# Optimization experiments

Measured on AMD Instinct MI355X. Metric: run time of the kernel, lower is better.

The kernel has to match this reference:

```python
import jax, jax.numpy as jnp
import numpy as np

T = 4096      # tokens
H = 1024      # hidden_size
I = 4096      # intermediate_size
E = 8         # num_experts


def setup_inputs() -> dict:
    key = jax.random.key(0)
    ks = jax.random.split(key, 6)
    s_h = 1.0 / np.sqrt(H)
    s_i = 1.0 / np.sqrt(I)
    return {
        "x":  jax.random.normal(ks[0], (T, H), dtype=jnp.float32),
        "Wg": jax.random.uniform(ks[1], (E, H), jnp.float32, -s_h, s_h),   # gate: Linear(H, E), no bias
        "W1": jax.random.uniform(ks[2], (E, H, I), jnp.float32, -s_h, s_h),
        "b1": jax.random.uniform(ks[3], (E, I), jnp.float32, -s_h, s_h),
        "W2": jax.random.uniform(ks[4], (E, I, H), jnp.float32, -s_i, s_i),
        "b2": jax.random.uniform(ks[5], (E, H), jnp.float32, -s_i, s_i),
    }


def reference(x, Wg, W1, b1, W2, b2):
    # Gate: softmax over experts. gate_scores: [T, E]
    gate_scores = jax.nn.softmax(x @ Wg.T, axis=-1)
    # All experts run densely on all tokens (batched GEMMs).
    h = jax.nn.gelu(jnp.einsum('th,ehi->eti', x, W1) + b1[:, None, :],
                    approximate=False)                      # [E, T, I]
    y = jnp.einsum('eti,eih->eth', h, W2) + b2[:, None, :]  # [E, T, H]
    # Gate-weighted sum over experts (fuses the stack + mul + sum).
    return jnp.einsum('te,eth->th', gate_scores, y)         # [T, H]
```

## Files before the change

kernel.cpp:

```cpp
#include <hip/hip_runtime.h>
#include <math.h>

#define T_TOK 4096
#define H_DIM 1024
#define I_DIM 4096
#define E_NUM 8


typedef short s16x8 __attribute__((ext_vector_type(8)));
typedef float f32x4 __attribute__((ext_vector_type(4)));

__device__ __forceinline__ unsigned short f2b(float f) {
  union { float f; unsigned u; } v; v.f = f;
  unsigned r = v.u + 0x7fffu + ((v.u >> 16) & 1u);
  return (unsigned short)(r >> 16);
}

__device__ __forceinline__ void gld_lds16(short* lds, const short* g) {
  __builtin_amdgcn_global_load_lds(
      (const __attribute__((address_space(1))) void*)g,
      (__attribute__((address_space(3))) void*)lds, 16, 0, 0);
}

__device__ __forceinline__ float gelu_f(float v) {
  float a = fabsf(v);
  float z = a * 0.70710678118f;
  float t = __builtin_amdgcn_rcpf(fmaf(0.47047f, z, 1.0f));
  float p = fmaf(fmaf(0.7478556f, t, -0.0958798f), t, 0.3480242f) * t;
  float e = __expf(-z * z);
  float erf_abs = fmaf(-p, e, 1.0f);
  return fmaf(0.5f * a, erf_abs, 0.5f * v);
}

__global__ __launch_bounds__(256) void gate_kernel(
    const float* __restrict__ x, const float* __restrict__ Wg,
    float* __restrict__ gate)
{
  int t = blockIdx.x * 4 + (threadIdx.x >> 6);
  int lane = threadIdx.x & 63;
  const float* xr = x + (size_t)t * H_DIM;
  float acc[E_NUM];
#pragma unroll
  for (int e = 0; e < E_NUM; ++e) acc[e] = 0.f;
  for (int j = 0; j < H_DIM / 64; ++j) {
    float xv = xr[lane + j * 64];
#pragma unroll
    for (int e = 0; e < E_NUM; ++e)
      acc[e] += xv * Wg[e * H_DIM + lane + j * 64];
  }
#pragma unroll
  for (int e = 0; e < E_NUM; ++e)
    for (int s = 32; s > 0; s >>= 1)
      acc[e] += __shfl_xor(acc[e], s, 64);
  if (lane == 0) {
    float mx = acc[0];
#pragma unroll
    for (int e = 1; e < E_NUM; ++e) mx = fmaxf(mx, acc[e]);
    float sum = 0.f, ex[E_NUM];
#pragma unroll
    for (int e = 0; e < E_NUM; ++e) { ex[e] = expf(acc[e] - mx); sum += ex[e]; }
    float inv = 1.f / sum;
#pragma unroll
    for (int e = 0; e < E_NUM; ++e) gate[t * E_NUM + e] = ex[e] * inv;
  }
}

__global__ __launch_bounds__(256) void convert_x_kernel(
    const float* __restrict__ x, short* __restrict__ xb)
{
  int idx = blockIdx.x * 256 + threadIdx.x;
  int t = idx >> 7;
  int h0 = (idx & 127) << 3;
  const float* src = x + (size_t)t * H_DIM + h0;
  float4 a = *(const float4*)src;
  float4 b = *(const float4*)(src + 4);
  s16x8 v;
  v[0] = f2b(a.x); v[1] = f2b(a.y); v[2] = f2b(a.z); v[3] = f2b(a.w);
  v[4] = f2b(b.x); v[5] = f2b(b.y); v[6] = f2b(b.z); v[7] = f2b(b.w);
  int rb = t >> 8, kt = h0 >> 6, half = (t >> 7) & 1;
  size_t off = ((size_t)((rb * 16 + kt) * 2 + half)) * 8192
             + (size_t)(t & 127) * 64 + (h0 & 63);
  *(s16x8*)(xb + off) = v;
}

__global__ __launch_bounds__(256) void trans_w1_kernel(
    const float* __restrict__ W1, short* __restrict__ W1t)
{
  __shared__ short tile[64][65];
  const int e = blockIdx.z;
  const int i0 = blockIdx.x * 64, h0 = blockIdx.y * 64;
  const int tid = threadIdx.x, c = tid & 63, r0 = tid >> 6;
  const float* src = W1 + ((size_t)e * H_DIM + h0) * I_DIM + i0;
#pragma unroll
  for (int j = 0; j < 16; ++j) {
    int r = j * 4 + r0;
    tile[r][c] = f2b(src[(size_t)r * I_DIM + c]);
  }
  __syncthreads();
  const int i = tid & 63, kq = tid >> 6;
  const size_t base = ((size_t)((e * 16 + (i0 >> 8)) * 16 + (h0 >> 6)) * 2
                       + ((i0 >> 7) & 1)) * 8192
                    + (size_t)((i0 & 64) + i) * 64;
#pragma unroll
  for (int w = 0; w < 2; ++w) {
    int kcl = kq + w * 4;
    s16x8 v;
#pragma unroll
    for (int j = 0; j < 8; ++j) v[j] = tile[kcl * 8 + j][i];
    *(s16x8*)(W1t + base + kcl * 8) = v;
  }
}

__global__ __launch_bounds__(256) void trans_w2_kernel(
    const float* __restrict__ W2, short* __restrict__ W2t)
{
  __shared__ short tile[64][65];
  const int e = blockIdx.z;
  const int i0 = blockIdx.x * 64, h0 = blockIdx.y * 64;
  const int tid = threadIdx.x, c = tid & 63, r0 = tid >> 6;
  const float* src = W2 + ((size_t)e * I_DIM + i0) * H_DIM + h0;
#pragma unroll
  for (int j = 0; j < 16; ++j) {
    int r = j * 4 + r0;
    tile[r][c] = f2b(src[(size_t)r * H_DIM + c]);
  }
  __syncthreads();
  const int h = tid & 63, kq = tid >> 6;
  const size_t base = ((size_t)((h0 >> 8) * 512 + e * 64 + (i0 >> 6)) * 2
                       + ((h0 >> 7) & 1)) * 8192
                    + (size_t)((h0 & 64) + h) * 64;
#pragma unroll
  for (int w = 0; w < 2; ++w) {
    int kcl = kq + w * 4;
    s16x8 v;
#pragma unroll
    for (int j = 0; j < 8; ++j) v[j] = tile[kcl * 8 + j][h];
    *(s16x8*)(W2t + base + kcl * 8) = v;
  }
}


#define BARR()  __builtin_amdgcn_s_barrier()
#define FENCE() asm volatile("" ::: "memory")
#define LGKM0() do { asm volatile("s_waitcnt lgkmcnt(0)" ::: "memory"); \
                     __builtin_amdgcn_sched_barrier(0); } while (0)
#define VMC(N)  asm volatile("s_waitcnt vmcnt(" #N ")" ::: "memory")
#define PRIO1() __builtin_amdgcn_s_setprio(1)
#define PRIO0() __builtin_amdgcn_s_setprio(0)
#define SCHEDB() __builtin_amdgcn_sched_barrier(0)

__device__ __forceinline__ void gemm_core(
    const short* __restrict__ Ag, const short* __restrict__ Bg,
    int nk, short* lds, f32x4 acc[8][4])
{
  const int tid  = threadIdx.x;
  const int wave = tid >> 6, lane = tid & 63;
  const int wm = wave >> 2, wn = wave & 3;
  const int g = lane >> 4, r16 = lane & 15;

  const int L0 = tid * 16;
  const int L1 = 8192 + tid * 16;
  const int s0 = (L0 ^ (((L0 >> 7) & 7) << 4)) >> 1;
  const int s1 = (L1 ^ (((L1 >> 7) & 7) << 4)) >> 1;

  short* stA = lds + wave * 512;
  short* stB = lds + 32768 + wave * 512;

  const int xr_ = (r16 & 7) << 4;
  const int rd0 = r16 * 64 + ((((0 << 6) | (g << 4)) ^ xr_) >> 1);
  const int rd1 = r16 * 64 + ((((1 << 6) | (g << 4)) ^ xr_) >> 1);

  const short* Ah = lds + wm * 8192;
  const short* Bh = lds + 32768 + (wn >> 1) * 8192 + (wn & 1) * 4096;

  s16x8 af[16], bf0, bf1;

#define STAGE_A(KT, HH, BUF) do { \
    const short* _s = Ag + (size_t)(KT) * 16384 + (HH) * 8192; \
    short* _d = stA + ((BUF) * 2 + (HH)) * 8192; \
    gld_lds16(_d, _s + s0); \
    gld_lds16(_d + 4096, _s + s1); } while (0)
#define STAGE_B(KT, HH, BUF) do { \
    const short* _s = Bg + (size_t)(KT) * 16384 + (HH) * 8192; \
    short* _d = stB + ((BUF) * 2 + (HH)) * 8192; \
    gld_lds16(_d, _s + s0); \
    gld_lds16(_d + 4096, _s + s1); } while (0)
#define LDA(BUF) \
    _Pragma("unroll") \
    for (int mi = 0; mi < 8; ++mi) { \
      af[mi * 2]     = *(const s16x8*)(Ah + (BUF) * 16384 + mi * 1024 + rd0); \
      af[mi * 2 + 1] = *(const s16x8*)(Ah + (BUF) * 16384 + mi * 1024 + rd1); }
#define LDB(BUF, NL) do { \
    bf0 = *(const s16x8*)(Bh + (BUF) * 16384 + (NL) * 1024 + rd0); \
    bf1 = *(const s16x8*)(Bh + (BUF) * 16384 + (NL) * 1024 + rd1); } while (0)
#define MFMA_COL(NL) \
    _Pragma("unroll") \
    for (int mi = 0; mi < 8; ++mi) { \
      acc[mi][NL] = __builtin_amdgcn_mfma_f32_16x16x32_bf16(af[mi * 2], bf0, acc[mi][NL], 0, 0, 0); \
      acc[mi][NL] = __builtin_amdgcn_mfma_f32_16x16x32_bf16(af[mi * 2 + 1], bf1, acc[mi][NL], 0, 0, 0); }

  STAGE_A(0, 0, 0); STAGE_A(0, 1, 0); STAGE_B(0, 0, 0); STAGE_B(0, 1, 0);
  STAGE_A(1, 0, 1); STAGE_A(1, 1, 1);
  VMC(4);
  BARR(); FENCE();

  const int iters = nk >> 1;
  for (int it = 0; it < iters; ++it) {
    const int u = it * 2, v = u + 1;
    const bool nlast = (it + 1 < iters);

    LDA(0); LDB(0, 0);
    STAGE_B(v, 0, 1);
    BARR(); LGKM0();
    PRIO1(); MFMA_COL(0); PRIO0();
    SCHEDB(); BARR(); FENCE();

    LDB(0, 1);
    STAGE_B(v, 1, 1);
    BARR(); LGKM0();
    PRIO1(); MFMA_COL(1); PRIO0();
    SCHEDB(); BARR(); FENCE();

    LDB(0, 2);
    if (nlast) STAGE_A(u + 2, 0, 0);
    BARR(); LGKM0();
    PRIO1(); MFMA_COL(2); PRIO0();
    SCHEDB(); BARR(); FENCE();

    LDB(0, 3);
    if (nlast) STAGE_A(u + 2, 1, 0);
    BARR(); LGKM0();
    PRIO1(); MFMA_COL(3); PRIO0();
    if (nlast) { VMC(4); } else { VMC(0); }
    SCHEDB(); BARR(); FENCE();

    LDA(1); LDB(1, 0);
    if (nlast) STAGE_B(u + 2, 0, 0);
    BARR(); LGKM0();
    PRIO1(); MFMA_COL(0); PRIO0();
    SCHEDB(); BARR(); FENCE();

    LDB(1, 1);
    if (nlast) STAGE_B(u + 2, 1, 0);
    BARR(); LGKM0();
    PRIO1(); MFMA_COL(1); PRIO0();
    SCHEDB(); BARR(); FENCE();

    LDB(1, 2);
    if (nlast) STAGE_A(v + 2, 0, 1);
    BARR(); LGKM0();
    PRIO1(); MFMA_COL(2); PRIO0();
    SCHEDB(); BARR(); FENCE();

    LDB(1, 3);
    if (nlast) STAGE_A(v + 2, 1, 1);
    BARR(); LGKM0();
    PRIO1(); MFMA_COL(3); PRIO0();
    if (nlast) VMC(4);
    SCHEDB(); BARR(); FENCE();
  }
#undef STAGE_A
#undef STAGE_B
#undef LDA
#undef LDB
#undef MFMA_COL
}

__global__ __launch_bounds__(512) void gemm1_kernel(
    const short* __restrict__ xb, const short* __restrict__ W1t,
    const float* __restrict__ b1, const float* __restrict__ gate,
    short* __restrict__ hg)
{
  extern __shared__ short lds[];
  const int bi = blockIdx.x, bt = blockIdx.y, e = blockIdx.z;
  f32x4 acc[8][4];
#pragma unroll
  for (int i = 0; i < 8; ++i)
#pragma unroll
    for (int j = 0; j < 4; ++j) acc[i][j] = (f32x4){0.f, 0.f, 0.f, 0.f};

  const short* Ag = W1t + (size_t)(e * 16 + bi) * 16 * 16384;
  const short* Bg = xb + (size_t)bt * 16 * 16384;
  gemm_core(Ag, Bg, 16, lds, acc);

  const int tid = threadIdx.x, wave = tid >> 6, lane = tid & 63;
  const int wm = wave >> 2, wn = wave & 3, g = lane >> 4, r16 = lane & 15;
#pragma unroll
  for (int mg = 0; mg < 8; ++mg) {
    const int i4 = bi * 256 + wm * 128 + mg * 16 + g * 4;
    const float4 b1v = *(const float4*)(b1 + e * I_DIM + i4);
    const int kt = (e * I_DIM + i4) >> 6;
    const int c = i4 & 63;
    short* dst = hg + ((size_t)(bt * 512 + kt) * 2 + (wn >> 1)) * 8192 + c;
#pragma unroll
    for (int ng = 0; ng < 4; ++ng) {
      const int tl = wn * 64 + ng * 16 + r16;
      const float gt = gate[(bt * 256 + tl) * E_NUM + e];
      const float v0 = gelu_f(acc[mg][ng][0] + b1v.x) * gt;
      const float v1 = gelu_f(acc[mg][ng][1] + b1v.y) * gt;
      const float v2 = gelu_f(acc[mg][ng][2] + b1v.z) * gt;
      const float v3 = gelu_f(acc[mg][ng][3] + b1v.w) * gt;
      int2 pk;
      pk.x = (int)((unsigned)f2b(v0) | ((unsigned)f2b(v1) << 16));
      pk.y = (int)((unsigned)f2b(v2) | ((unsigned)f2b(v3) << 16));
      *(int2*)(dst + (size_t)(tl & 127) * 64) = pk;
    }
  }
}

__global__ __launch_bounds__(512) void gemm2_kernel(
    const short* __restrict__ W2t, const short* __restrict__ hg,
    float* __restrict__ part)
{
  extern __shared__ short lds[];
  const int bh = blockIdx.x, bt = blockIdx.y, ks = blockIdx.z;
  f32x4 acc[8][4];
#pragma unroll
  for (int i = 0; i < 8; ++i)
#pragma unroll
    for (int j = 0; j < 4; ++j) acc[i][j] = (f32x4){0.f, 0.f, 0.f, 0.f};

  const short* Ag = W2t + (size_t)(bh * 512 + ks * 128) * 16384;
  const short* Bg = hg  + (size_t)(bt * 512 + ks * 128) * 16384;
  gemm_core(Ag, Bg, 128, lds, acc);

  const int tid = threadIdx.x, wave = tid >> 6, lane = tid & 63;
  const int wm = wave >> 2, wn = wave & 3, g = lane >> 4, r16 = lane & 15;
  float* dst = part + (size_t)ks * ((size_t)T_TOK * H_DIM);
#pragma unroll
  for (int mg = 0; mg < 8; ++mg) {
    const int h4 = bh * 256 + wm * 128 + mg * 16 + g * 4;
#pragma unroll
    for (int ng = 0; ng < 4; ++ng) {
      const int t = bt * 256 + wn * 64 + ng * 16 + r16;
      *(f32x4*)(dst + (size_t)t * H_DIM + h4) = acc[mg][ng];
    }
  }
}

__global__ __launch_bounds__(256) void reduce_kernel(
    const float* __restrict__ part, const float* __restrict__ gate,
    const float* __restrict__ b2, float* __restrict__ out)
{
  const int idx = blockIdx.x * 256 + threadIdx.x;
  const int t = idx >> 8;
  const int h4 = (idx & 255) << 2;
  const size_t off = (size_t)t * H_DIM + h4;
  const size_t SL = (size_t)T_TOK * H_DIM;
  float4 a0 = *(const float4*)(part + off);
  float4 a1 = *(const float4*)(part + SL + off);
  float4 a2 = *(const float4*)(part + 2 * SL + off);
  float4 a3 = *(const float4*)(part + 3 * SL + off);
  float sx = a0.x + a1.x + a2.x + a3.x;
  float sy = a0.y + a1.y + a2.y + a3.y;
  float sz = a0.z + a1.z + a2.z + a3.z;
  float sw = a0.w + a1.w + a2.w + a3.w;
#pragma unroll
  for (int e = 0; e < E_NUM; ++e) {
    const float gv = gate[t * E_NUM + e];
    const float4 bv = *(const float4*)(b2 + e * H_DIM + h4);
    sx = fmaf(gv, bv.x, sx); sy = fmaf(gv, bv.y, sy);
    sz = fmaf(gv, bv.z, sz); sw = fmaf(gv, bv.w, sw);
  }
  float4 r; r.x = sx; r.y = sy; r.z = sz; r.w = sw;
  *(float4*)(out + off) = r;
}

extern "C" void kernel_launch(void* const* d_in, const int* in_sizes, int n_in,
                              void* d_out, int out_size, void* d_ws, size_t ws_size,
                              hipStream_t stream) {
  const float* x  = (const float*)d_in[0];
  const float* Wg = (const float*)d_in[1];
  const float* W1 = (const float*)d_in[2];
  const float* b1 = (const float*)d_in[3];
  const float* W2 = (const float*)d_in[4];
  const float* b2 = (const float*)d_in[5];
  float* out = (float*)d_out;

  char* ws = (char*)d_ws;
  float* gate = (float*)ws;
  short* xb   = (short*)(ws + 131072);
  short* W1t  = (short*)(ws + 131072 + 8388608);
  short* W2t  = (short*)(ws + 131072 + 8388608 + 67108864);
  short* hg   = (short*)(ws + 131072 + 8388608 + 2 * 67108864);
  float* part = (float*)(ws + 131072);

  static bool attr_done = false;
  if (!attr_done) {
    hipFuncSetAttribute((const void*)gemm1_kernel,
                        hipFuncAttributeMaxDynamicSharedMemorySize, 131072);
    hipFuncSetAttribute((const void*)gemm2_kernel,
                        hipFuncAttributeMaxDynamicSharedMemorySize, 131072);
    attr_done = true;
  }

  gate_kernel<<<T_TOK / 4, 256, 0, stream>>>(x, Wg, gate);
  convert_x_kernel<<<2048, 256, 0, stream>>>(x, xb);
  trans_w1_kernel<<<dim3(I_DIM / 64, H_DIM / 64, E_NUM), 256, 0, stream>>>(W1, W1t);
  trans_w2_kernel<<<dim3(I_DIM / 64, H_DIM / 64, E_NUM), 256, 0, stream>>>(W2, W2t);
  gemm1_kernel<<<dim3(16, 16, 8), 512, 131072, stream>>>(xb, W1t, b1, gate, hg);
  gemm2_kernel<<<dim3(4, 16, 4), 512, 131072, stream>>>(W2t, hg, part);
  reduce_kernel<<<4096, 256, 0, stream>>>(part, gate, b2, out);
}
```

Baseline: 893.8 us.

## Rewrite GEMMs with 128x128 tiles, 4-stage pipeline, 2 blocks per CU

Replaces the 256x256, 512-thread GEMM core with 128x128 tiles over 256 threads and a k=32 packed layout. A 4-deep global-to-LDS ring buffer uses one barrier per k-step, and launch bounds allow two blocks per CU. All weight and activation transforms switch to 32-wide k chunks. gemm1 now loops over all experts inside one block, reusing the x tile from cache, and gemm2 drops split-K from 4 to 2, so the reduce kernel sums fewer partials. The intent is better occupancy and latency hiding, at the cost of lower per-block arithmetic intensity and more LDS traffic per MFMA.

```diff
diff --git a/kernel.cpp b/kernel.cpp
--- a/kernel.cpp
+++ b/kernel.cpp
@@ -77,9 +77,8 @@
   s16x8 v;
   v[0] = f2b(a.x); v[1] = f2b(a.y); v[2] = f2b(a.z); v[3] = f2b(a.w);
   v[4] = f2b(b.x); v[5] = f2b(b.y); v[6] = f2b(b.z); v[7] = f2b(b.w);
-  int rb = t >> 8, kt = h0 >> 6, half = (t >> 7) & 1;
-  size_t off = ((size_t)((rb * 16 + kt) * 2 + half)) * 8192
-             + (size_t)(t & 127) * 64 + (h0 & 63);
+  size_t off = ((size_t)((t >> 7) * 32 + (h0 >> 5))) * 4096
+             + (size_t)(t & 127) * 32 + (h0 & 31);
   *(s16x8*)(xb + off) = v;
 }
 
@@ -98,16 +97,15 @@
   }
   __syncthreads();
   const int i = tid & 63, kq = tid >> 6;
-  const size_t base = ((size_t)((e * 16 + (i0 >> 8)) * 16 + (h0 >> 6)) * 2
-                       + ((i0 >> 7) & 1)) * 8192
-                    + (size_t)((i0 & 64) + i) * 64;
 #pragma unroll
   for (int w = 0; w < 2; ++w) {
     int kcl = kq + w * 4;
     s16x8 v;
 #pragma unroll
     for (int j = 0; j < 8; ++j) v[j] = tile[kcl * 8 + j][i];
-    *(s16x8*)(W1t + base + kcl * 8) = v;
+    size_t off = (((size_t)e * 32 + (i0 >> 7)) * 32 + (h0 >> 5) + (kcl >> 2)) * 4096
+               + (size_t)((i0 & 64) + i) * 32 + (kcl & 3) * 8;
+    *(s16x8*)(W1t + off) = v;
   }
 }
 
@@ -126,16 +124,15 @@
   }
   __syncthreads();
   const int h = tid & 63, kq = tid >> 6;
-  const size_t base = ((size_t)((h0 >> 8) * 512 + e * 64 + (i0 >> 6)) * 2
-                       + ((h0 >> 7) & 1)) * 8192
-                    + (size_t)((h0 & 64) + h) * 64;
 #pragma unroll
   for (int w = 0; w < 2; ++w) {
     int kcl = kq + w * 4;
     s16x8 v;
 #pragma unroll
     for (int j = 0; j < 8; ++j) v[j] = tile[kcl * 8 + j][h];
-    *(s16x8*)(W2t + base + kcl * 8) = v;
+    size_t off = ((size_t)(h0 >> 7) * 1024 + e * 128 + (i0 >> 5) + (kcl >> 2)) * 4096
+               + (size_t)((h0 & 64) + h) * 32 + (kcl & 3) * 8;
+    *(s16x8*)(W2t + off) = v;
   }
 }
 
@@ -148,192 +145,178 @@
 #define PRIO1() __builtin_amdgcn_s_setprio(1)
 #define PRIO0() __builtin_amdgcn_s_setprio(0)
 #define SCHEDB() __builtin_amdgcn_sched_barrier(0)
-
-__device__ __forceinline__ void gemm_core(
-    const short* __restrict__ Ag, const short* __restrict__ Bg,
-    int nk, short* lds, f32x4 acc[8][4])
-{
-  const int tid  = threadIdx.x;
-  const int wave = tid >> 6, lane = tid & 63;
-  const int wm = wave >> 2, wn = wave & 3;
-  const int g = lane >> 4, r16 = lane & 15;
-
-  const int L0 = tid * 16;
-  const int L1 = 8192 + tid * 16;
-  const int s0 = (L0 ^ (((L0 >> 7) & 7) << 4)) >> 1;
-  const int s1 = (L1 ^ (((L1 >> 7) & 7) << 4)) >> 1;
-
-  short* stA = lds + wave * 512;
-  short* stB = lds + 32768 + wave * 512;
-
-  const int xr_ = (r16 & 7) << 4;
-  const int rd0 = r16 * 64 + ((((0 << 6) | (g << 4)) ^ xr_) >> 1);
-  const int rd1 = r16 * 64 + ((((1 << 6) | (g << 4)) ^ xr_) >> 1);
-
-  const short* Ah = lds + wm * 8192;
-  const short* Bh = lds + 32768 + (wn >> 1) * 8192 + (wn & 1) * 4096;
-
-  s16x8 af[16], bf0, bf1;
-
-#define STAGE_A(KT, HH, BUF) do { \
-    const short* _s = Ag + (size_t)(KT) * 16384 + (HH) * 8192; \
-    short* _d = stA + ((BUF) * 2 + (HH)) * 8192; \
-    gld_lds16(_d, _s + s0); \
-    gld_lds16(_d + 4096, _s + s1); } while (0)
-#define STAGE_B(KT, HH, BUF) do { \
-    const short* _s = Bg + (size_t)(KT) * 16384 + (HH) * 8192; \
-    short* _d = stB + ((BUF) * 2 + (HH)) * 8192; \
-    gld_lds16(_d, _s + s0); \
-    gld_lds16(_d + 4096, _s + s1); } while (0)
-#define LDA(BUF) \
-    _Pragma("unroll") \
-    for (int mi = 0; mi < 8; ++mi) { \
-      af[mi * 2]     = *(const s16x8*)(Ah + (BUF) * 16384 + mi * 1024 + rd0); \
-      af[mi * 2 + 1] = *(const s16x8*)(Ah + (BUF) * 16384 + mi * 1024 + rd1); }
-#define LDB(BUF, NL) do { \
-    bf0 = *(const s16x8*)(Bh + (BUF) * 16384 + (NL) * 1024 + rd0); \
-    bf1 = *(const s16x8*)(Bh + (BUF) * 16384 + (NL) * 1024 + rd1); } while (0)
-#define MFMA_COL(NL) \
-    _Pragma("unroll") \
-    for (int mi = 0; mi < 8; ++mi) { \
-      acc[mi][NL] = __builtin_amdgcn_mfma_f32_16x16x32_bf16(af[mi * 2], bf0, acc[mi][NL], 0, 0, 0); \
-      acc[mi][NL] = __builtin_amdgcn_mfma_f32_16x16x32_bf16(af[mi * 2 + 1], bf1, acc[mi][NL], 0, 0, 0); }
-
-  STAGE_A(0, 0, 0); STAGE_A(0, 1, 0); STAGE_B(0, 0, 0); STAGE_B(0, 1, 0);
-  STAGE_A(1, 0, 1); STAGE_A(1, 1, 1);
-  VMC(4);
-  BARR(); FENCE();
-
-  const int iters = nk >> 1;
-  for (int it = 0; it < iters; ++it) {
-    const int u = it * 2, v = u + 1;
-    const bool nlast = (it + 1 < iters);
-
-    LDA(0); LDB(0, 0);
-    STAGE_B(v, 0, 1);
-    BARR(); LGKM0();
-    PRIO1(); MFMA_COL(0); PRIO0();
-    SCHEDB(); BARR(); FENCE();
-
-    LDB(0, 1);
-    STAGE_B(v, 1, 1);
-    BARR(); LGKM0();
-    PRIO1(); MFMA_COL(1); PRIO0();
-    SCHEDB(); BARR(); FENCE();
-
-    LDB(0, 2);
-    if (nlast) STAGE_A(u + 2, 0, 0);
-    BARR(); LGKM0();
-    PRIO1(); MFMA_COL(2); PRIO0();
-    SCHEDB(); BARR(); FENCE();
-
-    LDB(0, 3);
-    if (nlast) STAGE_A(u + 2, 1, 0);
-    BARR(); LGKM0();
-    PRIO1(); MFMA_COL(3); PRIO0();
-    if (nlast) { VMC(4); } else { VMC(0); }
-    SCHEDB(); BARR(); FENCE();
-
-    LDA(1); LDB(1, 0);
-    if (nlast) STAGE_B(u + 2, 0, 0);
-    BARR(); LGKM0();
-    PRIO1(); MFMA_COL(0); PRIO0();
-    SCHEDB(); BARR(); FENCE();
-
-    LDB(1, 1);
-    if (nlast) STAGE_B(u + 2, 1, 0);
-    BARR(); LGKM0();
-    PRIO1(); MFMA_COL(1); PRIO0();
-    SCHEDB(); BARR(); FENCE();
-
-    LDB(1, 2);
-    if (nlast) STAGE_A(v + 2, 0, 1);
-    BARR(); LGKM0();
-    PRIO1(); MFMA_COL(2); PRIO0();
-    SCHEDB(); BARR(); FENCE();
-
-    LDB(1, 3);
-    if (nlast) STAGE_A(v + 2, 1, 1);
-    BARR(); LGKM0();
-    PRIO1(); MFMA_COL(3); PRIO0();
-    if (nlast) VMC(4);
-    SCHEDB(); BARR(); FENCE();
-  }
-#undef STAGE_A
-#undef STAGE_B
-#undef LDA
-#undef LDB
-#undef MFMA_COL
-}
-
-__global__ __launch_bounds__(512) void gemm1_kernel(
+#define MF(A, B, C) __builtin_amdgcn_mfma_f32_16x16x32_bf16(A, B, C, 0, 0, 0)
+
+__global__ __launch_bounds__(256, 2) void gemm1_kernel(
     const short* __restrict__ xb, const short* __restrict__ W1t,
     const float* __restrict__ b1, const float* __restrict__ gate,
     short* __restrict__ hg)
 {
   extern __shared__ short lds[];
-  const int bi = blockIdx.x, bt = blockIdx.y, e = blockIdx.z;
-  f32x4 acc[8][4];
-#pragma unroll
-  for (int i = 0; i < 8; ++i)
+  const int bi = blockIdx.x, bt = blockIdx.y;
+  const int tid = threadIdx.x, wave = tid >> 6, lane = tid & 63;
+  const int wm = wave >> 1, wn = wave & 1;
+  const int g = lane >> 4, r16 = lane & 15;
+
+  const int D0 = (wave * 2) * 1024 + lane * 16;
+  const int D1 = (wave * 2 + 1) * 1024 + lane * 16;
+  const int s0 = (D0 ^ (((D0 >> 6) & 3) << 4)) >> 1;
+  const int s1 = (D1 ^ (((D1 >> 6) & 3) << 4)) >> 1;
+  short* dA0 = lds + (wave * 2) * 512;
+  short* dA1 = lds + (wave * 2 + 1) * 512;
+  short* dB0 = lds + 16384 + (wave * 2) * 512;
+  short* dB1 = lds + 16384 + (wave * 2 + 1) * 512;
+
+  const int rdf = r16 * 32 + ((g << 3) ^ ((r16 & 3) << 3));
+  const short* Ah = lds + (wm * 64) * 32;
+  const short* Bh = lds + 16384 + (wn * 64) * 32;
+
+  const short* Bw = xb + (size_t)bt * 32 * 4096;
+
+  f32x4 acc[4][4];
+#pragma unroll
+  for (int i = 0; i < 4; ++i)
 #pragma unroll
     for (int j = 0; j < 4; ++j) acc[i][j] = (f32x4){0.f, 0.f, 0.f, 0.f};
 
-  const short* Ag = W1t + (size_t)(e * 16 + bi) * 16 * 16384;
-  const short* Bg = xb + (size_t)bt * 16 * 16384;
-  gemm_core(Ag, Bg, 16, lds, acc);
-
-  const int tid = threadIdx.x, wave = tid >> 6, lane = tid & 63;
-  const int wm = wave >> 2, wn = wave & 3, g = lane >> 4, r16 = lane & 15;
-#pragma unroll
-  for (int mg = 0; mg < 8; ++mg) {
-    const int i4 = bi * 256 + wm * 128 + mg * 16 + g * 4;
-    const float4 b1v = *(const float4*)(b1 + e * I_DIM + i4);
-    const int kt = (e * I_DIM + i4) >> 6;
-    const int c = i4 & 63;
-    short* dst = hg + ((size_t)(bt * 512 + kt) * 2 + (wn >> 1)) * 8192 + c;
-#pragma unroll
-    for (int ng = 0; ng < 4; ++ng) {
-      const int tl = wn * 64 + ng * 16 + r16;
-      const float gt = gate[(bt * 256 + tl) * E_NUM + e];
-      const float v0 = gelu_f(acc[mg][ng][0] + b1v.x) * gt;
-      const float v1 = gelu_f(acc[mg][ng][1] + b1v.y) * gt;
-      const float v2 = gelu_f(acc[mg][ng][2] + b1v.z) * gt;
-      const float v3 = gelu_f(acc[mg][ng][3] + b1v.w) * gt;
-      int2 pk;
-      pk.x = (int)((unsigned)f2b(v0) | ((unsigned)f2b(v1) << 16));
-      pk.y = (int)((unsigned)f2b(v2) | ((unsigned)f2b(v3) << 16));
-      *(int2*)(dst + (size_t)(tl & 127) * 64) = pk;
+#define STAGE1(KK) do { \
+    const int _c = ((KK) >> 5) * 1024 + bi * 32 + ((KK) & 31); \
+    const short* _sa = W1t + (size_t)_c * 4096; \
+    const short* _sb = Bw + (size_t)((KK) & 31) * 4096; \
+    const int _o = ((KK) & 3) * 4096; \
+    gld_lds16(dA0 + _o, _sa + s0); \
+    gld_lds16(dA1 + _o, _sa + s1); \
+    gld_lds16(dB0 + _o, _sb + s0); \
+    gld_lds16(dB1 + _o, _sb + s1); } while (0)
+
+  STAGE1(0); STAGE1(1); STAGE1(2);
+
+  for (int e = 0; e < E_NUM; ++e) {
+#pragma unroll 4
+    for (int t32 = 0; t32 < 32; ++t32) {
+      const int k = e * 32 + t32;
+      if (k < 254) { VMC(8); } else if (k == 254) { VMC(4); } else { VMC(0); }
+      BARR(); FENCE();
+      if (k + 3 < 256) STAGE1(k + 3);
+      const int o = (k & 3) * 4096;
+      s16x8 av[4], bv[4];
+#pragma unroll
+      for (int mi = 0; mi < 4; ++mi)
+        av[mi] = *(const s16x8*)(Ah + o + mi * 512 + rdf);
+#pragma unroll
+      for (int ni = 0; ni < 4; ++ni)
+        bv[ni] = *(const s16x8*)(Bh + o + ni * 512 + rdf);
+      LGKM0();
+      PRIO1();
+#pragma unroll
+      for (int mi = 0; mi < 4; ++mi)
+#pragma unroll
+        for (int ni = 0; ni < 4; ++ni)
+          acc[mi][ni] = MF(av[mi], bv[ni], acc[mi][ni]);
+      PRIO0(); SCHEDB();
     }
-  }
-}
-
-__global__ __launch_bounds__(512) void gemm2_kernel(
+
+#pragma unroll
+    for (int mi = 0; mi < 4; ++mi) {
+      const int i4 = bi * 128 + wm * 64 + mi * 16 + g * 4;
+      const float4 b1v = *(const float4*)(b1 + e * I_DIM + i4);
+      const int kt32 = (e * I_DIM + i4) >> 5;
+      const int col = i4 & 31;
+      short* dst = hg + ((size_t)bt * 1024 + kt32) * 4096 + col;
+#pragma unroll
+      for (int ni = 0; ni < 4; ++ni) {
+        const int tl = wn * 64 + ni * 16 + r16;
+        const float gt = gate[(bt * 128 + tl) * E_NUM + e];
+        const float v0 = gelu_f(acc[mi][ni][0] + b1v.x) * gt;
+        const float v1 = gelu_f(acc[mi][ni][1] + b1v.y) * gt;
+        const float v2 = gelu_f(acc[mi][ni][2] + b1v.z) * gt;
+        const float v3 = gelu_f(acc[mi][ni][3] + b1v.w) * gt;
+        int2 pk;
+        pk.x = (int)((unsigned)f2b(v0) | ((unsigned)f2b(v1) << 16));
+        pk.y = (int)((unsigned)f2b(v2) | ((unsigned)f2b(v3) << 16));
+        *(int2*)(dst + (size_t)tl * 32) = pk;
+        acc[mi][ni] = (f32x4){0.f, 0.f, 0.f, 0.f};
+      }
+    }
+  }
+#undef STAGE1
+}
+
+__global__ __launch_bounds__(256, 2) void gemm2_kernel(
     const short* __restrict__ W2t, const short* __restrict__ hg,
     float* __restrict__ part)
 {
   extern __shared__ short lds[];
   const int bh = blockIdx.x, bt = blockIdx.y, ks = blockIdx.z;
-  f32x4 acc[8][4];
-#pragma unroll
-  for (int i = 0; i < 8; ++i)
+  const int tid = threadIdx.x, wave = tid >> 6, lane = tid & 63;
+  const int wm = wave >> 1, wn = wave & 1;
+  const int g = lane >> 4, r16 = lane & 15;
+
+  const int D0 = (wave * 2) * 1024 + lane * 16;
+  const int D1 = (wave * 2 + 1) * 1024 + lane * 16;
+  const int s0 = (D0 ^ (((D0 >> 6) & 3) << 4)) >> 1;
+  const int s1 = (D1 ^ (((D1 >> 6) & 3) << 4)) >> 1;
+  short* dA0 = lds + (wave * 2) * 512;
+  short* dA1 = lds + (wave * 2 + 1) * 512;
+  short* dB0 = lds + 16384 + (wave * 2) * 512;
+  short* dB1 = lds + 16384 + (wave * 2 + 1) * 512;
+
+  const int rdf = r16 * 32 + ((g << 3) ^ ((r16 & 3) << 3));
+  const short* Ah = lds + (wm * 64) * 32;
+  const short* Bh = lds + 16384 + (wn * 64) * 32;
+
+  const short* Aw = W2t + ((size_t)bh * 1024 + ks * 512) * 4096;
+  const short* Bw = hg + ((size_t)bt * 1024 + ks * 512) * 4096;
+
+  f32x4 acc[4][4];
+#pragma unroll
+  for (int i = 0; i < 4; ++i)
 #pragma unroll
     for (int j = 0; j < 4; ++j) acc[i][j] = (f32x4){0.f, 0.f, 0.f, 0.f};
 
-  const short* Ag = W2t + (size_t)(bh * 512 + ks * 128) * 16384;
-  const short* Bg = hg  + (size_t)(bt * 512 + ks * 128) * 16384;
-  gemm_core(Ag, Bg, 128, lds, acc);
-
-  const int tid = threadIdx.x, wave = tid >> 6, lane = tid & 63;
-  const int wm = wave >> 2, wn = wave & 3, g = lane >> 4, r16 = lane & 15;
+#define STAGE2(KK) do { \
+    const short* _sa = Aw + (size_t)(KK) * 4096; \
+    const short* _sb = Bw + (size_t)(KK) * 4096; \
+    const int _o = ((KK) & 3) * 4096; \
+    gld_lds16(dA0 + _o, _sa + s0); \
+    gld_lds16(dA1 + _o, _sa + s1); \
+    gld_lds16(dB0 + _o, _sb + s0); \
+    gld_lds16(dB1 + _o, _sb + s1); } while (0)
+
+  STAGE2(0); STAGE2(1); STAGE2(2);
+
+#pragma unroll 4
+  for (int k = 0; k < 512; ++k) {
+    if (k < 510) { VMC(8); } else if (k == 510) { VMC(4); } else { VMC(0); }
+    BARR(); FENCE();
+    if (k + 3 < 512) STAGE2(k + 3);
+    const int o = (k & 3) * 4096;
+    s16x8 av[4], bv[4];
+#pragma unroll
+    for (int mi = 0; mi < 4; ++mi)
+      av[mi] = *(const s16x8*)(Ah + o + mi * 512 + rdf);
+#pragma unroll
+    for (int ni = 0; ni < 4; ++ni)
+      bv[ni] = *(const s16x8*)(Bh + o + ni * 512 + rdf);
+    LGKM0();
+    PRIO1();
+#pragma unroll
+    for (int mi = 0; mi < 4; ++mi)
+#pragma unroll
+      for (int ni = 0; ni < 4; ++ni)
+        acc[mi][ni] = MF(av[mi], bv[ni], acc[mi][ni]);
+    PRIO0(); SCHEDB();
+  }
+#undef STAGE2
+
   float* dst = part + (size_t)ks * ((size_t)T_TOK * H_DIM);
 #pragma unroll
-  for (int mg = 0; mg < 8; ++mg) {
-    const int h4 = bh * 256 + wm * 128 + mg * 16 + g * 4;
-#pragma unroll
-    for (int ng = 0; ng < 4; ++ng) {
-      const int t = bt * 256 + wn * 64 + ng * 16 + r16;
-      *(f32x4*)(dst + (size_t)t * H_DIM + h4) = acc[mg][ng];
+  for (int mi = 0; mi < 4; ++mi) {
+    const int h4 = bh * 128 + wm * 64 + mi * 16 + g * 4;
+#pragma unroll
+    for (int ni = 0; ni < 4; ++ni) {
+      const int t = bt * 128 + wn * 64 + ni * 16 + r16;
+      *(f32x4*)(dst + (size_t)t * H_DIM + h4) = acc[mi][ni];
     }
   }
 }
@@ -349,12 +332,10 @@
   const size_t SL = (size_t)T_TOK * H_DIM;
   float4 a0 = *(const float4*)(part + off);
   float4 a1 = *(const float4*)(part + SL + off);
-  float4 a2 = *(const float4*)(part + 2 * SL + off);
-  float4 a3 = *(const float4*)(part + 3 * SL + off);
-  float sx = a0.x + a1.x + a2.x + a3.x;
-  float sy = a0.y + a1.y + a2.y + a3.y;
-  float sz = a0.z + a1.z + a2.z + a3.z;
-  float sw = a0.w + a1.w + a2.w + a3.w;
+  float sx = a0.x + a1.x;
+  float sy = a0.y + a1.y;
+  float sz = a0.z + a1.z;
+  float sw = a0.w + a1.w;
 #pragma unroll
   for (int e = 0; e < E_NUM; ++e) {
     const float gv = gate[t * E_NUM + e];
@@ -388,9 +369,9 @@
   static bool attr_done = false;
   if (!attr_done) {
     hipFuncSetAttribute((const void*)gemm1_kernel,
-                        hipFuncAttributeMaxDynamicSharedMemorySize, 131072);
+                        hipFuncAttributeMaxDynamicSharedMemorySize, 65536);
     hipFuncSetAttribute((const void*)gemm2_kernel,
-                        hipFuncAttributeMaxDynamicSharedMemorySize, 131072);
+                        hipFuncAttributeMaxDynamicSharedMemorySize, 65536);
     attr_done = true;
   }
 
@@ -398,7 +379,7 @@
   convert_x_kernel<<<2048, 256, 0, stream>>>(x, xb);
   trans_w1_kernel<<<dim3(I_DIM / 64, H_DIM / 64, E_NUM), 256, 0, stream>>>(W1, W1t);
   trans_w2_kernel<<<dim3(I_DIM / 64, H_DIM / 64, E_NUM), 256, 0, stream>>>(W2, W2t);
-  gemm1_kernel<<<dim3(16, 16, 8), 512, 131072, stream>>>(xb, W1t, b1, gate, hg);
-  gemm2_kernel<<<dim3(4, 16, 4), 512, 131072, stream>>>(W2t, hg, part);
+  gemm1_kernel<<<dim3(32, 32), 256, 65536, stream>>>(xb, W1t, b1, gate, hg);
+  gemm2_kernel<<<dim3(8, 32, 2), 256, 65536, stream>>>(W2t, hg, part);
   reduce_kernel<<<4096, 256, 0, stream>>>(part, gate, b2, out);
 }
```

New measurement: 980.0 us. 9.6% more time.
